# Optimization experiments

Hardware: AMD Instinct MI355X
Metric: run time of the kernel (lower is better)

## Reference

```python
import jax, jax.numpy as jnp
import numpy as np

NUM_HEADS = 8
OUT_DIM = 32


def setup_inputs() -> dict:
    key = jax.random.key(0)
    k1, k2, k3, k4 = jax.random.split(key, 4)
    B, N, IN = 2048, 64, 256
    h_i_list = jax.random.normal(k1, (B, N, IN), dtype=jnp.float32)
    h_j_list = jax.random.normal(k2, (B, N, IN), dtype=jnp.float32)
    # Linear weight, applied as x @ W (in_dim, num_heads*out_dim)
    W = jax.random.normal(k3, (IN, NUM_HEADS * OUT_DIM), dtype=jnp.float32) * (1.0 / np.sqrt(IN))
    W_att = jax.random.normal(k4, (1, NUM_HEADS, OUT_DIM), dtype=jnp.float32) * 0.1
    return {"h_i_list": h_i_list, "h_j_list": h_j_list, "W": W, "W_att": W_att}


def reference(h_i_list, h_j_list, W, W_att):
    B, N, _ = h_i_list.shape
    H, D = NUM_HEADS, OUT_DIM
    # [B, N, H, D]
    proj_neigh = (h_j_list @ W).reshape(B, N, H, D)
    proj_self = (h_i_list @ W).reshape(B, N, H, D)
    # attention logits: leakyReLU(sum over feature dim) -> [B, N, H]
    e_ij = jax.nn.leaky_relu(((proj_neigh + proj_self) * W_att[None]).sum(-1), 0.2)
    # softmax over neighbor dim (dim=1)
    alpha = jax.nn.softmax(e_ij, axis=1)  # [B, N, H]
    # weighted neighbor sum -> [B, H, D]
    weight_sum = jnp.einsum("bnh,bnhd->bhd", alpha, proj_neigh)
    # concat=True: [B, 1, H*D]
    h_new = weight_sum.reshape(B, 1, H * D)
    return jax.nn.elu(h_new)
```

## Files before the change

kernel.cpp:

```cpp
#include <hip/hip_runtime.h>

#define NN 64
#define IND 256
#define NH 8
#define OD 32

typedef __attribute__((ext_vector_type(8))) short bf16x8;
typedef __attribute__((ext_vector_type(4))) float f32x4;

__device__ __forceinline__ unsigned f2bf(float f) {
  unsigned u = __float_as_uint(f);
  return (u + (((u >> 16) & 1u) + 0x7fffu)) >> 16;
}

__global__ __launch_bounds__(256) void precompute_v(
    const float* __restrict__ W, const float* __restrict__ Watt, float* __restrict__ V) {
  int tid = blockIdx.x * 256 + threadIdx.x;
  if (tid >= IND * NH) return;
  int h = tid >> 8, k = tid & 255;
  float acc = 0.f;
#pragma unroll
  for (int d = 0; d < OD; ++d) acc += W[k * 256 + h * OD + d] * Watt[h * OD + d];
  V[h * 256 + k] = acc;
}

#define V_OFF 33792
#define E_OFF (V_OFF + 4224)
#define SMEM_BYTES (E_OFF + 2304)

__global__ __launch_bounds__(256) void gat_fused(
    const float* __restrict__ Xi, const float* __restrict__ Xj,
    const float* __restrict__ W, const float* __restrict__ V,
    float* __restrict__ out) {
  __shared__ __align__(16) unsigned char smem[SMEM_BYTES];
  unsigned* s_pk = (unsigned*)smem;
  unsigned* v_pk = (unsigned*)(smem + V_OFF);
  float* e_f = (float*)(smem + E_OFF);
  float* alpha_f = (float*)(smem + V_OFF);
  float* pp_f = (float*)(smem + V_OFF);
  float* yp_f = (float*)smem;

  const int t = threadIdx.x;
  const int b = blockIdx.x;
  const int w = t >> 6, l = t & 63;
  const int g = l >> 3, h = l & 7;

  const float4* Xi4 = (const float4*)Xi + (size_t)b * (NN * IND / 4) + w * 1024;
  const float4* Xj4 = (const float4*)Xj + (size_t)b * (NN * IND / 4) + w * 1024;

  {
    const float4* V4 = (const float4*)V;
#pragma unroll
    for (int r = 0; r < 8; ++r) {
      float4 vv = V4[r * 64 + l];
      unsigned p0 = f2bf(vv.x) | (f2bf(vv.y) << 16);
      unsigned p1 = f2bf(vv.z) | (f2bf(vv.w) << 16);
      *(uint2*)(v_pk + r * 132 + 2 * l) = make_uint2(p0, p1);
    }
  }

  float4 xj[16];
#pragma unroll
  for (int i = 0; i < 16; ++i) xj[i] = Xj4[i * 64 + l];
#pragma unroll
  for (int c = 0; c < 2; ++c) {
    float4 xi[8];
#pragma unroll
    for (int i = 0; i < 8; ++i) xi[i] = Xi4[(c * 8 + i) * 64 + l];
#pragma unroll
    for (int i = 0; i < 8; ++i) {
      int r = c * 8 + i;
      float4 a = xj[r], ci = xi[i];
      unsigned p0 = f2bf(a.x + ci.x) | (f2bf(a.y + ci.y) << 16);
      unsigned p1 = f2bf(a.z + ci.z) | (f2bf(a.w + ci.w) << 16);
      *(uint2*)(s_pk + (w * 16 + r) * 132 + l * 2) = make_uint2(p0, p1);
    }
  }

  {
    const int r16 = l & 15, q = l >> 4;
    const unsigned* arow = s_pk + (w * 16 + r16) * 132;
    const unsigned* brow = v_pk + (r16 & 7) * 132;
    f32x4 acc = {0.f, 0.f, 0.f, 0.f};
#pragma unroll
    for (int step = 0; step < 8; ++step) {
      bf16x8 af = *(const bf16x8*)(arow + step * 16 + q * 4);
      bf16x8 bfv = *(const bf16x8*)(brow + step * 16 + q * 4);
      acc = __builtin_amdgcn_mfma_f32_16x16x32_bf16(af, bfv, acc, 0, 0, 0);
    }
    if (r16 < 8) {
#pragma unroll
      for (int j = 0; j < 4; ++j) {
        float ev = acc[j];
        ev = ev >= 0.f ? ev : 0.2f * ev;
        e_f[(w * 16 + q * 4 + j) * 9 + r16] = ev;
      }
    }
  }
  __syncthreads();

  float m = -3.4e38f;
#pragma unroll
  for (int q = 0; q < 8; ++q) m = fmaxf(m, e_f[(g * 8 + q) * 9 + h]);
  m = fmaxf(m, __shfl_xor(m, 8, 64));
  m = fmaxf(m, __shfl_xor(m, 16, 64));
  m = fmaxf(m, __shfl_xor(m, 32, 64));
  float ssum = 0.f;
#pragma unroll
  for (int q = 0; q < 8; ++q) ssum += __expf(e_f[(g * 8 + q) * 9 + h] - m);
  ssum += __shfl_xor(ssum, 8, 64);
  ssum += __shfl_xor(ssum, 16, 64);
  ssum += __shfl_xor(ssum, 32, 64);
  float rinv = 1.f / ssum;

#pragma unroll
  for (int pp = 0; pp < 2; ++pp) {
    int n = w * 16 + g + 8 * pp;
    alpha_f[n * 8 + h] = __expf(e_f[n * 9 + h] - m) * rinv;
  }

  float4 acc4[8];
#pragma unroll
  for (int hh = 0; hh < 8; ++hh) acc4[hh] = make_float4(0.f, 0.f, 0.f, 0.f);
#pragma unroll
  for (int i = 0; i < 16; ++i) {
    int n = w * 16 + i;
    float4 a0 = *(const float4*)(alpha_f + n * 8);
    float4 a1 = *(const float4*)(alpha_f + n * 8 + 4);
    float al[8] = {a0.x, a0.y, a0.z, a0.w, a1.x, a1.y, a1.z, a1.w};
    float4 x = xj[i];
#pragma unroll
    for (int hh = 0; hh < 8; ++hh) {
      acc4[hh].x += al[hh] * x.x;
      acc4[hh].y += al[hh] * x.y;
      acc4[hh].z += al[hh] * x.z;
      acc4[hh].w += al[hh] * x.w;
    }
  }
#pragma unroll
  for (int hh = 0; hh < 8; ++hh)
    *(float4*)(yp_f + (w * 8 + hh) * 260 + 4 * l) = acc4[hh];
  __syncthreads();

#pragma unroll
  for (int c = 0; c < 2; ++c) {
    int id = t + c * 256;
    int row = id >> 6, col = (id & 63) * 4;
    float* p = yp_f + row * 260 + col;
    float4 s0 = *(float4*)p;
    float4 s1 = *(float4*)(p + 2080);
    float4 s2 = *(float4*)(p + 4160);
    float4 s3 = *(float4*)(p + 6240);
    s0.x += s1.x + s2.x + s3.x;
    s0.y += s1.y + s2.y + s3.y;
    s0.z += s1.z + s2.z + s3.z;
    s0.w += s1.w + s2.w + s3.w;
    *(float4*)p = s0;
  }
  __syncthreads();

  {
    const float* ypb = yp_f + g * 260;
    const float4* W4 = (const float4*)W;
    float4 acc = make_float4(0.f, 0.f, 0.f, 0.f);
    int k0 = w * 64;
#pragma unroll 8
    for (int kc = 0; kc < 16; ++kc) {
      int k = k0 + kc * 4;
      float4 yv = *(const float4*)(ypb + k);
      float4 w0 = W4[(k + 0) * 64 + l];
      float4 w1 = W4[(k + 1) * 64 + l];
      float4 w2 = W4[(k + 2) * 64 + l];
      float4 w3 = W4[(k + 3) * 64 + l];
      acc.x += yv.x * w0.x + yv.y * w1.x + yv.z * w2.x + yv.w * w3.x;
      acc.y += yv.x * w0.y + yv.y * w1.y + yv.z * w2.y + yv.w * w3.y;
      acc.z += yv.x * w0.z + yv.y * w1.z + yv.z * w2.z + yv.w * w3.z;
      acc.w += yv.x * w0.w + yv.y * w1.w + yv.z * w2.w + yv.w * w3.w;
    }
    *(float4*)(pp_f + w * 256 + 4 * l) = acc;
  }
  __syncthreads();

  {
    float s = pp_f[t] + pp_f[256 + t] + pp_f[512 + t] + pp_f[768 + t];
    out[(size_t)b * 256 + t] = s > 0.f ? s : (__expf(s) - 1.f);
  }
}

extern "C" void kernel_launch(void* const* d_in, const int* in_sizes, int n_in,
                              void* d_out, int out_size, void* d_ws, size_t ws_size,
                              hipStream_t stream) {
  const float* Xi = (const float*)d_in[0];
  const float* Xj = (const float*)d_in[1];
  const float* W = (const float*)d_in[2];
  const float* Watt = (const float*)d_in[3];
  float* out = (float*)d_out;
  float* V = (float*)d_ws;
  int B = in_sizes[0] / (NN * IND);
  precompute_v<<<(IND * NH + 255) / 256, 256, 0, stream>>>(W, Watt, V);
  gat_fused<<<B, 256, 0, stream>>>(Xi, Xj, W, V, out);
}
```

Before: 285.0 us.

## Process two batches per block and prefetch the second batch's Xj during the first

Each block now handles two batch elements, b and b+grid, and the grid is halved. The Xj registers for the second batch are loaded partway through the first batch's work, so the global-memory latency overlaps the reduction and projection stages. The cost is doubled Xj register storage (another 64 floats per thread), which can lower occupancy or cause spills. The second batch also runs serially within the block and is followed by an extra barrier.

```diff
diff --git a/kernel.cpp b/kernel.cpp
--- a/kernel.cpp
+++ b/kernel.cpp
@@ -28,10 +28,35 @@
 #define E_OFF (V_OFF + 4224)
 #define SMEM_BYTES (E_OFF + 2304)
 
+#define STAGE_V()                                                     \
+  {                                                                   \
+    const float4* V4 = (const float4*)V;                              \
+    _Pragma("unroll") for (int r = 0; r < 8; ++r) {                   \
+      float4 vv = V4[r * 64 + l];                                     \
+      unsigned p0 = f2bf(vv.x) | (f2bf(vv.y) << 16);                  \
+      unsigned p1 = f2bf(vv.z) | (f2bf(vv.w) << 16);                  \
+      *(uint2*)(v_pk + r * 132 + 2 * l) = make_uint2(p0, p1);         \
+    }                                                                 \
+  }
+
+#define PACK_S(XI4, XJ)                                               \
+  _Pragma("unroll") for (int c = 0; c < 2; ++c) {                     \
+    float4 xi[8];                                                     \
+    _Pragma("unroll") for (int i = 0; i < 8; ++i)                     \
+        xi[i] = (XI4)[(c * 8 + i) * 64 + l];                          \
+    _Pragma("unroll") for (int i = 0; i < 8; ++i) {                   \
+      int r = c * 8 + i;                                              \
+      float4 a = (XJ)[r], ci = xi[i];                                 \
+      unsigned p0 = f2bf(a.x + ci.x) | (f2bf(a.y + ci.y) << 16);      \
+      unsigned p1 = f2bf(a.z + ci.z) | (f2bf(a.w + ci.w) << 16);      \
+      *(uint2*)(s_pk + (w * 16 + r) * 132 + l * 2) = make_uint2(p0, p1); \
+    }                                                                 \
+  }
+
 __global__ __launch_bounds__(256) void gat_fused(
     const float* __restrict__ Xi, const float* __restrict__ Xj,
     const float* __restrict__ W, const float* __restrict__ V,
-    float* __restrict__ out) {
+    float* __restrict__ out, int nB) {
   __shared__ __align__(16) unsigned char smem[SMEM_BYTES];
   unsigned* s_pk = (unsigned*)smem;
   unsigned* v_pk = (unsigned*)(smem + V_OFF);
@@ -41,149 +66,257 @@
   float* yp_f = (float*)smem;
 
   const int t = threadIdx.x;
-  const int b = blockIdx.x;
   const int w = t >> 6, l = t & 63;
   const int g = l >> 3, h = l & 7;
 
-  const float4* Xi4 = (const float4*)Xi + (size_t)b * (NN * IND / 4) + w * 1024;
-  const float4* Xj4 = (const float4*)Xj + (size_t)b * (NN * IND / 4) + w * 1024;
+  const int b0 = blockIdx.x;
+  const int b1 = blockIdx.x + gridDim.x;
+  const bool has2 = (b1 < nB);
+
+  const float4* Xi4a = (const float4*)Xi + (size_t)b0 * (NN * IND / 4) + w * 1024;
+  const float4* Xj4a = (const float4*)Xj + (size_t)b0 * (NN * IND / 4) + w * 1024;
+  const float4* Xi4b = (const float4*)Xi + (size_t)b1 * (NN * IND / 4) + w * 1024;
+  const float4* Xj4b = (const float4*)Xj + (size_t)b1 * (NN * IND / 4) + w * 1024;
+
+  float4 xjA[16], xjB[16];
+
+  STAGE_V();
+#pragma unroll
+  for (int i = 0; i < 16; ++i) xjA[i] = Xj4a[i * 64 + l];
+  PACK_S(Xi4a, xjA);
 
   {
-    const float4* V4 = (const float4*)V;
-#pragma unroll
-    for (int r = 0; r < 8; ++r) {
-      float4 vv = V4[r * 64 + l];
-      unsigned p0 = f2bf(vv.x) | (f2bf(vv.y) << 16);
-      unsigned p1 = f2bf(vv.z) | (f2bf(vv.w) << 16);
-      *(uint2*)(v_pk + r * 132 + 2 * l) = make_uint2(p0, p1);
+    {
+      const int r16 = l & 15, q = l >> 4;
+      const unsigned* arow = s_pk + (w * 16 + r16) * 132;
+      const unsigned* brow = v_pk + (r16 & 7) * 132;
+      f32x4 acc = {0.f, 0.f, 0.f, 0.f};
+#pragma unroll
+      for (int step = 0; step < 8; ++step) {
+        bf16x8 af = *(const bf16x8*)(arow + step * 16 + q * 4);
+        bf16x8 bfv = *(const bf16x8*)(brow + step * 16 + q * 4);
+        acc = __builtin_amdgcn_mfma_f32_16x16x32_bf16(af, bfv, acc, 0, 0, 0);
+      }
+      if (r16 < 8) {
+#pragma unroll
+        for (int j = 0; j < 4; ++j) {
+          float ev = acc[j];
+          ev = ev >= 0.f ? ev : 0.2f * ev;
+          e_f[(w * 16 + q * 4 + j) * 9 + r16] = ev;
+        }
+      }
+    }
+    __syncthreads();
+
+    float m = -3.4e38f;
+#pragma unroll
+    for (int q = 0; q < 8; ++q) m = fmaxf(m, e_f[(g * 8 + q) * 9 + h]);
+    m = fmaxf(m, __shfl_xor(m, 8, 64));
+    m = fmaxf(m, __shfl_xor(m, 16, 64));
+    m = fmaxf(m, __shfl_xor(m, 32, 64));
+    float ssum = 0.f;
+#pragma unroll
+    for (int q = 0; q < 8; ++q) ssum += __expf(e_f[(g * 8 + q) * 9 + h] - m);
+    ssum += __shfl_xor(ssum, 8, 64);
+    ssum += __shfl_xor(ssum, 16, 64);
+    ssum += __shfl_xor(ssum, 32, 64);
+    float rinv = 1.f / ssum;
+#pragma unroll
+    for (int pp = 0; pp < 2; ++pp) {
+      int n = w * 16 + g + 8 * pp;
+      alpha_f[n * 8 + h] = __expf(e_f[n * 9 + h] - m) * rinv;
+    }
+
+    float4 acc4[8];
+#pragma unroll
+    for (int hh = 0; hh < 8; ++hh) acc4[hh] = make_float4(0.f, 0.f, 0.f, 0.f);
+#pragma unroll
+    for (int i = 0; i < 16; ++i) {
+      int n = w * 16 + i;
+      float4 a0 = *(const float4*)(alpha_f + n * 8);
+      float4 a1 = *(const float4*)(alpha_f + n * 8 + 4);
+      float al[8] = {a0.x, a0.y, a0.z, a0.w, a1.x, a1.y, a1.z, a1.w};
+      float4 x = xjA[i];
+#pragma unroll
+      for (int hh = 0; hh < 8; ++hh) {
+        acc4[hh].x += al[hh] * x.x;
+        acc4[hh].y += al[hh] * x.y;
+        acc4[hh].z += al[hh] * x.z;
+        acc4[hh].w += al[hh] * x.w;
+      }
+    }
+
+    if (has2) {
+#pragma unroll
+      for (int i = 0; i < 16; ++i) xjB[i] = Xj4b[i * 64 + l];
+      __builtin_amdgcn_sched_barrier(0);
+    }
+
+#pragma unroll
+    for (int hh = 0; hh < 8; ++hh)
+      *(float4*)(yp_f + (w * 8 + hh) * 260 + 4 * l) = acc4[hh];
+    __syncthreads();
+
+#pragma unroll
+    for (int c = 0; c < 2; ++c) {
+      int id = t + c * 256;
+      int row = id >> 6, col = (id & 63) * 4;
+      float* p = yp_f + row * 260 + col;
+      float4 s0 = *(float4*)p;
+      float4 s1 = *(float4*)(p + 2080);
+      float4 s2 = *(float4*)(p + 4160);
+      float4 s3 = *(float4*)(p + 6240);
+      s0.x += s1.x + s2.x + s3.x;
+      s0.y += s1.y + s2.y + s3.y;
+      s0.z += s1.z + s2.z + s3.z;
+      s0.w += s1.w + s2.w + s3.w;
+      *(float4*)p = s0;
+    }
+    __syncthreads();
+
+    {
+      const float* ypb = yp_f + g * 260;
+      const float4* W4 = (const float4*)W;
+      float4 acc = make_float4(0.f, 0.f, 0.f, 0.f);
+      int k0 = w * 64;
+#pragma unroll 8
+      for (int kc = 0; kc < 16; ++kc) {
+        int k = k0 + kc * 4;
+        float4 yv = *(const float4*)(ypb + k);
+        float4 w0 = W4[(k + 0) * 64 + l];
+        float4 w1 = W4[(k + 1) * 64 + l];
+        float4 w2 = W4[(k + 2) * 64 + l];
+        float4 w3 = W4[(k + 3) * 64 + l];
+        acc.x += yv.x * w0.x + yv.y * w1.x + yv.z * w2.x + yv.w * w3.x;
+        acc.y += yv.x * w0.y + yv.y * w1.y + yv.z * w2.y + yv.w * w3.y;
+        acc.z += yv.x * w0.z + yv.y * w1.z + yv.z * w2.z + yv.w * w3.z;
+        acc.w += yv.x * w0.w + yv.y * w1.w + yv.z * w2.w + yv.w * w3.w;
+      }
+      *(float4*)(pp_f + w * 256 + 4 * l) = acc;
+    }
+    __syncthreads();
+
+    {
+      float s = pp_f[t] + pp_f[256 + t] + pp_f[512 + t] + pp_f[768 + t];
+      out[(size_t)b0 * 256 + t] = s > 0.f ? s : (__expf(s) - 1.f);
     }
   }
 
-  float4 xj[16];
-#pragma unroll
-  for (int i = 0; i < 16; ++i) xj[i] = Xj4[i * 64 + l];
-#pragma unroll
-  for (int c = 0; c < 2; ++c) {
-    float4 xi[8];
-#pragma unroll
-    for (int i = 0; i < 8; ++i) xi[i] = Xi4[(c * 8 + i) * 64 + l];
-#pragma unroll
-    for (int i = 0; i < 8; ++i) {
-      int r = c * 8 + i;
-      float4 a = xj[r], ci = xi[i];
-      unsigned p0 = f2bf(a.x + ci.x) | (f2bf(a.y + ci.y) << 16);
-      unsigned p1 = f2bf(a.z + ci.z) | (f2bf(a.w + ci.w) << 16);
-      *(uint2*)(s_pk + (w * 16 + r) * 132 + l * 2) = make_uint2(p0, p1);
-    }
-  }
+  if (!has2) return;
+
+  __syncthreads();
+
+  STAGE_V();
+  PACK_S(Xi4b, xjB);
 
   {
-    const int r16 = l & 15, q = l >> 4;
-    const unsigned* arow = s_pk + (w * 16 + r16) * 132;
-    const unsigned* brow = v_pk + (r16 & 7) * 132;
-    f32x4 acc = {0.f, 0.f, 0.f, 0.f};
-#pragma unroll
-    for (int step = 0; step < 8; ++step) {
-      bf16x8 af = *(const bf16x8*)(arow + step * 16 + q * 4);
-      bf16x8 bfv = *(const bf16x8*)(brow + step * 16 + q * 4);
-      acc = __builtin_amdgcn_mfma_f32_16x16x32_bf16(af, bfv, acc, 0, 0, 0);
-    }
-    if (r16 < 8) {
-#pragma unroll
-      for (int j = 0; j < 4; ++j) {
-        float ev = acc[j];
-        ev = ev >= 0.f ? ev : 0.2f * ev;
-        e_f[(w * 16 + q * 4 + j) * 9 + r16] = ev;
-      }
-    }
-  }
-  __syncthreads();
-
-  float m = -3.4e38f;
-#pragma unroll
-  for (int q = 0; q < 8; ++q) m = fmaxf(m, e_f[(g * 8 + q) * 9 + h]);
-  m = fmaxf(m, __shfl_xor(m, 8, 64));
-  m = fmaxf(m, __shfl_xor(m, 16, 64));
-  m = fmaxf(m, __shfl_xor(m, 32, 64));
-  float ssum = 0.f;
-#pragma unroll
-  for (int q = 0; q < 8; ++q) ssum += __expf(e_f[(g * 8 + q) * 9 + h] - m);
-  ssum += __shfl_xor(ssum, 8, 64);
-  ssum += __shfl_xor(ssum, 16, 64);
-  ssum += __shfl_xor(ssum, 32, 64);
-  float rinv = 1.f / ssum;
-
-#pragma unroll
-  for (int pp = 0; pp < 2; ++pp) {
-    int n = w * 16 + g + 8 * pp;
-    alpha_f[n * 8 + h] = __expf(e_f[n * 9 + h] - m) * rinv;
-  }
-
-  float4 acc4[8];
-#pragma unroll
-  for (int hh = 0; hh < 8; ++hh) acc4[hh] = make_float4(0.f, 0.f, 0.f, 0.f);
-#pragma unroll
-  for (int i = 0; i < 16; ++i) {
-    int n = w * 16 + i;
-    float4 a0 = *(const float4*)(alpha_f + n * 8);
-    float4 a1 = *(const float4*)(alpha_f + n * 8 + 4);
-    float al[8] = {a0.x, a0.y, a0.z, a0.w, a1.x, a1.y, a1.z, a1.w};
-    float4 x = xj[i];
-#pragma unroll
-    for (int hh = 0; hh < 8; ++hh) {
-      acc4[hh].x += al[hh] * x.x;
-      acc4[hh].y += al[hh] * x.y;
-      acc4[hh].z += al[hh] * x.z;
-      acc4[hh].w += al[hh] * x.w;
-    }
-  }
-#pragma unroll
-  for (int hh = 0; hh < 8; ++hh)
-    *(float4*)(yp_f + (w * 8 + hh) * 260 + 4 * l) = acc4[hh];
-  __syncthreads();
-
-#pragma unroll
-  for (int c = 0; c < 2; ++c) {
-    int id = t + c * 256;
-    int row = id >> 6, col = (id & 63) * 4;
-    float* p = yp_f + row * 260 + col;
-    float4 s0 = *(float4*)p;
-    float4 s1 = *(float4*)(p + 2080);
-    float4 s2 = *(float4*)(p + 4160);
-    float4 s3 = *(float4*)(p + 6240);
-    s0.x += s1.x + s2.x + s3.x;
-    s0.y += s1.y + s2.y + s3.y;
-    s0.z += s1.z + s2.z + s3.z;
-    s0.w += s1.w + s2.w + s3.w;
-    *(float4*)p = s0;
-  }
-  __syncthreads();
-
-  {
-    const float* ypb = yp_f + g * 260;
-    const float4* W4 = (const float4*)W;
-    float4 acc = make_float4(0.f, 0.f, 0.f, 0.f);
-    int k0 = w * 64;
+    {
+      const int r16 = l & 15, q = l >> 4;
+      const unsigned* arow = s_pk + (w * 16 + r16) * 132;
+      const unsigned* brow = v_pk + (r16 & 7) * 132;
+      f32x4 acc = {0.f, 0.f, 0.f, 0.f};
+#pragma unroll
+      for (int step = 0; step < 8; ++step) {
+        bf16x8 af = *(const bf16x8*)(arow + step * 16 + q * 4);
+        bf16x8 bfv = *(const bf16x8*)(brow + step * 16 + q * 4);
+        acc = __builtin_amdgcn_mfma_f32_16x16x32_bf16(af, bfv, acc, 0, 0, 0);
+      }
+      if (r16 < 8) {
+#pragma unroll
+        for (int j = 0; j < 4; ++j) {
+          float ev = acc[j];
+          ev = ev >= 0.f ? ev : 0.2f * ev;
+          e_f[(w * 16 + q * 4 + j) * 9 + r16] = ev;
+        }
+      }
+    }
+    __syncthreads();
+
+    float m = -3.4e38f;
+#pragma unroll
+    for (int q = 0; q < 8; ++q) m = fmaxf(m, e_f[(g * 8 + q) * 9 + h]);
+    m = fmaxf(m, __shfl_xor(m, 8, 64));
+    m = fmaxf(m, __shfl_xor(m, 16, 64));
+    m = fmaxf(m, __shfl_xor(m, 32, 64));
+    float ssum = 0.f;
+#pragma unroll
+    for (int q = 0; q < 8; ++q) ssum += __expf(e_f[(g * 8 + q) * 9 + h] - m);
+    ssum += __shfl_xor(ssum, 8, 64);
+    ssum += __shfl_xor(ssum, 16, 64);
+    ssum += __shfl_xor(ssum, 32, 64);
+    float rinv = 1.f / ssum;
+#pragma unroll
+    for (int pp = 0; pp < 2; ++pp) {
+      int n = w * 16 + g + 8 * pp;
+      alpha_f[n * 8 + h] = __expf(e_f[n * 9 + h] - m) * rinv;
+    }
+
+    float4 acc4[8];
+#pragma unroll
+    for (int hh = 0; hh < 8; ++hh) acc4[hh] = make_float4(0.f, 0.f, 0.f, 0.f);
+#pragma unroll
+    for (int i = 0; i < 16; ++i) {
+      int n = w * 16 + i;
+      float4 a0 = *(const float4*)(alpha_f + n * 8);
+      float4 a1 = *(const float4*)(alpha_f + n * 8 + 4);
+      float al[8] = {a0.x, a0.y, a0.z, a0.w, a1.x, a1.y, a1.z, a1.w};
+      float4 x = xjB[i];
+#pragma unroll
+      for (int hh = 0; hh < 8; ++hh) {
+        acc4[hh].x += al[hh] * x.x;
+        acc4[hh].y += al[hh] * x.y;
+        acc4[hh].z += al[hh] * x.z;
+        acc4[hh].w += al[hh] * x.w;
+      }
+    }
+#pragma unroll
+    for (int hh = 0; hh < 8; ++hh)
+      *(float4*)(yp_f + (w * 8 + hh) * 260 + 4 * l) = acc4[hh];
+    __syncthreads();
+
+#pragma unroll
+    for (int c = 0; c < 2; ++c) {
+      int id = t + c * 256;
+      int row = id >> 6, col = (id & 63) * 4;
+      float* p = yp_f + row * 260 + col;
+      float4 s0 = *(float4*)p;
+      float4 s1 = *(float4*)(p + 2080);
+      float4 s2 = *(float4*)(p + 4160);
+      float4 s3 = *(float4*)(p + 6240);
+      s0.x += s1.x + s2.x + s3.x;
+      s0.y += s1.y + s2.y + s3.y;
+      s0.z += s1.z + s2.z + s3.z;
+      s0.w += s1.w + s2.w + s3.w;
+      *(float4*)p = s0;
+    }
+    __syncthreads();
+
+    {
+      const float* ypb = yp_f + g * 260;
+      const float4* W4 = (const float4*)W;
+      float4 acc = make_float4(0.f, 0.f, 0.f, 0.f);
+      int k0 = w * 64;
 #pragma unroll 8
-    for (int kc = 0; kc < 16; ++kc) {
-      int k = k0 + kc * 4;
-      float4 yv = *(const float4*)(ypb + k);
-      float4 w0 = W4[(k + 0) * 64 + l];
-      float4 w1 = W4[(k + 1) * 64 + l];
-      float4 w2 = W4[(k + 2) * 64 + l];
-      float4 w3 = W4[(k + 3) * 64 + l];
-      acc.x += yv.x * w0.x + yv.y * w1.x + yv.z * w2.x + yv.w * w3.x;
-      acc.y += yv.x * w0.y + yv.y * w1.y + yv.z * w2.y + yv.w * w3.y;
-      acc.z += yv.x * w0.z + yv.y * w1.z + yv.z * w2.z + yv.w * w3.z;
-      acc.w += yv.x * w0.w + yv.y * w1.w + yv.z * w2.w + yv.w * w3.w;
-    }
-    *(float4*)(pp_f + w * 256 + 4 * l) = acc;
-  }
-  __syncthreads();
-
-  {
-    float s = pp_f[t] + pp_f[256 + t] + pp_f[512 + t] + pp_f[768 + t];
-    out[(size_t)b * 256 + t] = s > 0.f ? s : (__expf(s) - 1.f);
+      for (int kc = 0; kc < 16; ++kc) {
+        int k = k0 + kc * 4;
+        float4 yv = *(const float4*)(ypb + k);
+        float4 w0 = W4[(k + 0) * 64 + l];
+        float4 w1 = W4[(k + 1) * 64 + l];
+        float4 w2 = W4[(k + 2) * 64 + l];
+        float4 w3 = W4[(k + 3) * 64 + l];
+        acc.x += yv.x * w0.x + yv.y * w1.x + yv.z * w2.x + yv.w * w3.x;
+        acc.y += yv.x * w0.y + yv.y * w1.y + yv.z * w2.y + yv.w * w3.y;
+        acc.z += yv.x * w0.z + yv.y * w1.z + yv.z * w2.z + yv.w * w3.z;
+        acc.w += yv.x * w0.w + yv.y * w1.w + yv.z * w2.w + yv.w * w3.w;
+      }
+      *(float4*)(pp_f + w * 256 + 4 * l) = acc;
+    }
+    __syncthreads();
+
+    {
+      float s = pp_f[t] + pp_f[256 + t] + pp_f[512 + t] + pp_f[768 + t];
+      out[(size_t)b1 * 256 + t] = s > 0.f ? s : (__expf(s) - 1.f);
+    }
   }
 }
 
@@ -198,5 +331,6 @@
   float* V = (float*)d_ws;
   int B = in_sizes[0] / (NN * IND);
   precompute_v<<<(IND * NH + 255) / 256, 256, 0, stream>>>(W, Watt, V);
-  gat_fused<<<B, 256, 0, stream>>>(Xi, Xj, W, V, out);
+  int grid = (B + 1) / 2;
+  gat_fused<<<grid, 256, 0, stream>>>(Xi, Xj, W, V, out, B);
 }
```

Measured after the change: 307.8 us. +8.0%, slower.

## Shrink LDS footprint and register pressure by staging GAT per-wave chunks

Applied to the files above, without the earlier changes.

Cuts shared memory from about 40KB to about 23KB by staging the summed bf16 rows per wave in two halves along the feature dimension, with the MFMA logit computation interleaved between halves. The Xj tile is no longer held in 16 registers across the softmax; it is reloaded from global memory (likely hitting cache) for the alpha-weighted sum. The final projection is split into two passes over head halves, which fuses the cross-wave reduction into the W matmul. The aim is higher occupancy, at the cost of a second read of Xj and extra barriers.

```diff
diff --git a/kernel.cpp b/kernel.cpp
--- a/kernel.cpp
+++ b/kernel.cpp
@@ -24,16 +24,16 @@
   V[h * 256 + k] = acc;
 }
 
-#define V_OFF 33792
-#define E_OFF (V_OFF + 4224)
-#define SMEM_BYTES (E_OFF + 2304)
+#define V_OFF 16896
+#define E_OFF 21120
+#define SMEM_BYTES 23424
 
 __global__ __launch_bounds__(256) void gat_fused(
     const float* __restrict__ Xi, const float* __restrict__ Xj,
     const float* __restrict__ W, const float* __restrict__ V,
     float* __restrict__ out) {
   __shared__ __align__(16) unsigned char smem[SMEM_BYTES];
-  unsigned* s_pk = (unsigned*)smem;
+  unsigned* s_w = (unsigned*)smem;
   unsigned* v_pk = (unsigned*)(smem + V_OFF);
   float* e_f = (float*)(smem + E_OFF);
   float* alpha_f = (float*)(smem + V_OFF);
@@ -44,9 +44,11 @@
   const int b = blockIdx.x;
   const int w = t >> 6, l = t & 63;
   const int g = l >> 3, h = l & 7;
-
-  const float4* Xi4 = (const float4*)Xi + (size_t)b * (NN * IND / 4) + w * 1024;
-  const float4* Xj4 = (const float4*)Xj + (size_t)b * (NN * IND / 4) + w * 1024;
+  const int fq = l >> 4, r16 = l & 15;
+
+  const float4* Xi4 = (const float4*)Xi + (size_t)b * (NN * IND / 4);
+  const float4* Xj4 = (const float4*)Xj + (size_t)b * (NN * IND / 4);
+  unsigned* ws = s_w + w * 1056;
 
   {
     const float4* V4 = (const float4*)V;
@@ -59,41 +61,44 @@
     }
   }
 
-  float4 xj[16];
-#pragma unroll
-  for (int i = 0; i < 16; ++i) xj[i] = Xj4[i * 64 + l];
+  f32x4 acc = {0.f, 0.f, 0.f, 0.f};
 #pragma unroll
   for (int c = 0; c < 2; ++c) {
-    float4 xi[8];
-#pragma unroll
-    for (int i = 0; i < 8; ++i) xi[i] = Xi4[(c * 8 + i) * 64 + l];
-#pragma unroll
-    for (int i = 0; i < 8; ++i) {
-      int r = c * 8 + i;
-      float4 a = xj[r], ci = xi[i];
-      unsigned p0 = f2bf(a.x + ci.x) | (f2bf(a.y + ci.y) << 16);
-      unsigned p1 = f2bf(a.z + ci.z) | (f2bf(a.w + ci.w) << 16);
-      *(uint2*)(s_pk + (w * 16 + r) * 132 + l * 2) = make_uint2(p0, p1);
-    }
-  }
-
+#pragma unroll
+    for (int bq = 0; bq < 2; ++bq) {
+      float4 xi[4], xj[4];
+#pragma unroll
+      for (int p = 0; p < 4; ++p) {
+        int pr = bq * 4 + p;
+        int f4 = (w * 16 + 2 * pr + (l >> 5)) * 64 + 32 * c + (l & 31);
+        xi[p] = Xi4[f4];
+        xj[p] = Xj4[f4];
+      }
+#pragma unroll
+      for (int p = 0; p < 4; ++p) {
+        int pr = bq * 4 + p;
+        int row = 2 * pr + (l >> 5);
+        float4 a = xj[p], ci = xi[p];
+        unsigned p0 = f2bf(a.x + ci.x) | (f2bf(a.y + ci.y) << 16);
+        unsigned p1 = f2bf(a.z + ci.z) | (f2bf(a.w + ci.w) << 16);
+        *(uint2*)(ws + row * 66 + 2 * (l & 31)) = make_uint2(p0, p1);
+      }
+    }
+#pragma unroll
+    for (int j = 0; j < 4; ++j) {
+      bf16x8 af = *(const bf16x8*)(ws + r16 * 66 + 16 * j + 4 * fq);
+      bf16x8 bv = *(const bf16x8*)(v_pk + (r16 & 7) * 132 + 64 * c + 16 * j + 4 * fq);
+      acc = __builtin_amdgcn_mfma_f32_16x16x32_bf16(af, bv, acc, 0, 0, 0);
+    }
+    if (c == 0) __builtin_amdgcn_sched_barrier(0);
+  }
   {
-    const int r16 = l & 15, q = l >> 4;
-    const unsigned* arow = s_pk + (w * 16 + r16) * 132;
-    const unsigned* brow = v_pk + (r16 & 7) * 132;
-    f32x4 acc = {0.f, 0.f, 0.f, 0.f};
-#pragma unroll
-    for (int step = 0; step < 8; ++step) {
-      bf16x8 af = *(const bf16x8*)(arow + step * 16 + q * 4);
-      bf16x8 bfv = *(const bf16x8*)(brow + step * 16 + q * 4);
-      acc = __builtin_amdgcn_mfma_f32_16x16x32_bf16(af, bfv, acc, 0, 0, 0);
-    }
     if (r16 < 8) {
 #pragma unroll
       for (int j = 0; j < 4; ++j) {
         float ev = acc[j];
         ev = ev >= 0.f ? ev : 0.2f * ev;
-        e_f[(w * 16 + q * 4 + j) * 9 + r16] = ev;
+        e_f[(w * 16 + fq * 4 + j) * 9 + r16] = ev;
       }
     }
   }
@@ -123,67 +128,75 @@
 #pragma unroll
   for (int hh = 0; hh < 8; ++hh) acc4[hh] = make_float4(0.f, 0.f, 0.f, 0.f);
 #pragma unroll
-  for (int i = 0; i < 16; ++i) {
-    int n = w * 16 + i;
-    float4 a0 = *(const float4*)(alpha_f + n * 8);
-    float4 a1 = *(const float4*)(alpha_f + n * 8 + 4);
-    float al[8] = {a0.x, a0.y, a0.z, a0.w, a1.x, a1.y, a1.z, a1.w};
-    float4 x = xj[i];
-#pragma unroll
-    for (int hh = 0; hh < 8; ++hh) {
-      acc4[hh].x += al[hh] * x.x;
-      acc4[hh].y += al[hh] * x.y;
-      acc4[hh].z += al[hh] * x.z;
-      acc4[hh].w += al[hh] * x.w;
-    }
-  }
-#pragma unroll
-  for (int hh = 0; hh < 8; ++hh)
-    *(float4*)(yp_f + (w * 8 + hh) * 260 + 4 * l) = acc4[hh];
-  __syncthreads();
-
-#pragma unroll
-  for (int c = 0; c < 2; ++c) {
-    int id = t + c * 256;
-    int row = id >> 6, col = (id & 63) * 4;
-    float* p = yp_f + row * 260 + col;
-    float4 s0 = *(float4*)p;
-    float4 s1 = *(float4*)(p + 2080);
-    float4 s2 = *(float4*)(p + 4160);
-    float4 s3 = *(float4*)(p + 6240);
-    s0.x += s1.x + s2.x + s3.x;
-    s0.y += s1.y + s2.y + s3.y;
-    s0.z += s1.z + s2.z + s3.z;
-    s0.w += s1.w + s2.w + s3.w;
-    *(float4*)p = s0;
-  }
-  __syncthreads();
+  for (int gr = 0; gr < 4; ++gr) {
+    float4 xr[4];
+#pragma unroll
+    for (int i2 = 0; i2 < 4; ++i2)
+      xr[i2] = Xj4[(w * 16 + 4 * gr + i2) * 64 + l];
+#pragma unroll
+    for (int i2 = 0; i2 < 4; ++i2) {
+      int n = w * 16 + 4 * gr + i2;
+      float4 a0 = *(const float4*)(alpha_f + n * 8);
+      float4 a1 = *(const float4*)(alpha_f + n * 8 + 4);
+      float al[8] = {a0.x, a0.y, a0.z, a0.w, a1.x, a1.y, a1.z, a1.w};
+      float4 x = xr[i2];
+#pragma unroll
+      for (int hh = 0; hh < 8; ++hh) {
+        acc4[hh].x += al[hh] * x.x;
+        acc4[hh].y += al[hh] * x.y;
+        acc4[hh].z += al[hh] * x.z;
+        acc4[hh].w += al[hh] * x.w;
+      }
+    }
+  }
 
   {
-    const float* ypb = yp_f + g * 260;
-    const float4* W4 = (const float4*)W;
-    float4 acc = make_float4(0.f, 0.f, 0.f, 0.f);
-    int k0 = w * 64;
-#pragma unroll 8
-    for (int kc = 0; kc < 16; ++kc) {
-      int k = k0 + kc * 4;
-      float4 yv = *(const float4*)(ypb + k);
-      float4 w0 = W4[(k + 0) * 64 + l];
-      float4 w1 = W4[(k + 1) * 64 + l];
-      float4 w2 = W4[(k + 2) * 64 + l];
-      float4 w3 = W4[(k + 3) * 64 + l];
-      acc.x += yv.x * w0.x + yv.y * w1.x + yv.z * w2.x + yv.w * w3.x;
-      acc.y += yv.x * w0.y + yv.y * w1.y + yv.z * w2.y + yv.w * w3.y;
-      acc.z += yv.x * w0.z + yv.y * w1.z + yv.z * w2.z + yv.w * w3.z;
-      acc.w += yv.x * w0.w + yv.y * w1.w + yv.z * w2.w + yv.w * w3.w;
-    }
-    *(float4*)(pp_f + w * 256 + 4 * l) = acc;
-  }
-  __syncthreads();
-
-  {
-    float s = pp_f[t] + pp_f[256 + t] + pp_f[512 + t] + pp_f[768 + t];
-    out[(size_t)b * 256 + t] = s > 0.f ? s : (__expf(s) - 1.f);
+    const int q4 = t & 31, kp = t >> 5;
+#pragma unroll
+    for (int P = 0; P < 2; ++P) {
+#pragma unroll
+      for (int p = 0; p < 4; ++p)
+        *(float4*)(yp_f + (w * 4 + p) * 260 + 4 * l) = acc4[4 * P + p];
+      __syncthreads();
+
+      {
+        int hh = q4 >> 3;
+        const float* yb = yp_f + hh * 260 + 32 * kp;
+        const float4* W4 = (const float4*)W;
+        float4 a = make_float4(0.f, 0.f, 0.f, 0.f);
+#pragma unroll
+        for (int j = 0; j < 8; ++j) {
+          float4 y0 = *(const float4*)(yb + 4 * j);
+          float4 y1 = *(const float4*)(yb + 1040 + 4 * j);
+          float4 y2 = *(const float4*)(yb + 2080 + 4 * j);
+          float4 y3 = *(const float4*)(yb + 3120 + 4 * j);
+          float4 yq;
+          yq.x = y0.x + y1.x + y2.x + y3.x;
+          yq.y = y0.y + y1.y + y2.y + y3.y;
+          yq.z = y0.z + y1.z + y2.z + y3.z;
+          yq.w = y0.w + y1.w + y2.w + y3.w;
+          int k = 32 * kp + 4 * j;
+          float4 w0 = W4[(k + 0) * 64 + 32 * P + q4];
+          float4 w1 = W4[(k + 1) * 64 + 32 * P + q4];
+          float4 w2 = W4[(k + 2) * 64 + 32 * P + q4];
+          float4 w3 = W4[(k + 3) * 64 + 32 * P + q4];
+          a.x += yq.x * w0.x + yq.y * w1.x + yq.z * w2.x + yq.w * w3.x;
+          a.y += yq.x * w0.y + yq.y * w1.y + yq.z * w2.y + yq.w * w3.y;
+          a.z += yq.x * w0.z + yq.y * w1.z + yq.z * w2.z + yq.w * w3.z;
+          a.w += yq.x * w0.w + yq.y * w1.w + yq.z * w2.w + yq.w * w3.w;
+        }
+        *(float4*)(pp_f + kp * 132 + 4 * q4) = a;
+      }
+      __syncthreads();
+
+      if (t < 128) {
+        float s = 0.f;
+#pragma unroll
+        for (int k8 = 0; k8 < 8; ++k8) s += pp_f[k8 * 132 + t];
+        out[(size_t)b * 256 + 128 * P + t] = s > 0.f ? s : (__expf(s) - 1.f);
+      }
+      if (P == 0) __syncthreads();
+    }
   }
 }
 
```

Result: slower. 303.8 us (+6.6%).
